# Kernel tuning notes

Hardware: AMD Instinct MI355X
Metric: run time of the kernel (lower is better)

Reference implementation:

```python
import jax, jax.numpy as jnp
import numpy as np

VOCAB, EMB, HID = 120000, 64, 128
B, T = 256, 512


def _rnn_layer(inp, W_ih, b_ih, W_hh, b_hh):
    # inp: [B,T,D]. PyTorch RNN: h_t = tanh(W_ih x_t + b_ih + W_hh h_{t-1} + b_hh)
    pre = jnp.einsum('btd,hd->bth', inp, W_ih) + b_ih + b_hh  # input part hoisted out of scan
    h0 = jnp.zeros((inp.shape[0], W_hh.shape[0]), inp.dtype)

    def step(h, p_t):
        h = jnp.tanh(p_t + h @ W_hh.T)
        return h, h

    hT, outs = jax.lax.scan(step, h0, pre.transpose(1, 0, 2))  # scan over time
    return outs.transpose(1, 0, 2), hT  # [B,T,H], [B,H]


def _layernorm(x, g, b, eps=1e-5):
    mu = jnp.mean(x, axis=-1, keepdims=True)
    var = jnp.var(x, axis=-1, keepdims=True)
    return (x - mu) * jax.lax.rsqrt(var + eps) * g + b


def setup_inputs() -> dict:
    key = jax.random.key(0)
    ks = jax.random.split(key, 10)
    emb = jax.random.normal(ks[0], (VOCAB, EMB), jnp.float32) * 0.02
    emb = emb.at[0].set(0.0)  # padding_idx=0
    s_in, s_h = 1.0 / np.sqrt(HID), 1.0 / np.sqrt(HID)
    return {
        'x': jax.random.randint(ks[1], (B, T), 0, VOCAB),
        'emb': emb,
        'W_ih1': jax.random.normal(ks[2], (HID, EMB), jnp.float32) * s_in,
        'b_ih1': jnp.zeros((HID,), jnp.float32),
        'W_hh1': jax.random.normal(ks[3], (HID, HID), jnp.float32) * s_h,
        'b_hh1': jnp.zeros((HID,), jnp.float32),
        'W_ih2': jax.random.normal(ks[4], (HID, HID), jnp.float32) * s_in,
        'b_ih2': jnp.zeros((HID,), jnp.float32),
        'W_hh2': jax.random.normal(ks[5], (HID, HID), jnp.float32) * s_h,
        'b_hh2': jnp.zeros((HID,), jnp.float32),
        'ln_g': jnp.ones((HID,), jnp.float32),
        'ln_b': jnp.zeros((HID,), jnp.float32),
        'proj_W': jax.random.normal(ks[6], (HID, HID), jnp.float32) * s_h,
        'proj_b': jnp.zeros((HID,), jnp.float32),
        'on_g': jnp.ones((HID,), jnp.float32),
        'on_b': jnp.zeros((HID,), jnp.float32),
    }


def reference(x, emb, W_ih1, b_ih1, W_hh1, b_hh1, W_ih2, b_ih2, W_hh2, b_hh2,
              ln_g, ln_b, proj_W, proj_b, on_g, on_b):
    e = emb[x]                                   # [B,T,64]
    out1, _ = _rnn_layer(e, W_ih1, b_ih1, W_hh1, b_hh1)   # dropout is identity in eval
    _, h2 = _rnn_layer(out1, W_ih2, b_ih2, W_hh2, b_hh2)  # h2: [B,128] (last hidden state)
    rep = _layernorm(h2, ln_g, ln_b)
    rep = jnp.tanh(rep @ proj_W.T + proj_b)
    rep = _layernorm(rep, on_g, on_b)
    return rep
```

## Files before the change

### kernel.cpp

```cpp
#include <hip/hip_runtime.h>

#define BT (256*512)
#define HID 128
#define EMB 64
#define CH 32

typedef _Float16 half2_t __attribute__((ext_vector_type(2)));

__device__ inline float fast_tanh(float x) {
    float e = __expf(2.f * x);
    return 1.f - __fdividef(2.f, e + 1.f);
}

#define OPQ(v) asm volatile("" : "+v"(v.x), "+v"(v.y), "+v"(v.z), "+v"(v.w))
#define W16PIN \
    OPQ(w0);OPQ(w1);OPQ(w2);OPQ(w3);OPQ(w4);OPQ(w5);OPQ(w6);OPQ(w7); \
    OPQ(w8);OPQ(w9);OPQ(w10);OPQ(w11);OPQ(w12);OPQ(w13);OPQ(w14);OPQ(w15);
#define WDUALLOAD \
    float4 w0=wr0[0],w1=wr0[1],w2=wr0[2],w3=wr0[3],w4=wr0[4],w5=wr0[5],w6=wr0[6],w7=wr0[7], \
           w8=wr1[0],w9=wr1[1],w10=wr1[2],w11=wr1[3],w12=wr1[4],w13=wr1[5],w14=wr1[6],w15=wr1[7];

#define DACC(n, m) { float4 hv = hp[n]; \
    a0=fmaf(hv.x,w##n.x,a0); a1=fmaf(hv.y,w##n.y,a1); \
    a2=fmaf(hv.z,w##n.z,a2); a3=fmaf(hv.w,w##n.w,a3); \
    c0=fmaf(hv.x,w##m.x,c0); c1=fmaf(hv.y,w##m.y,c1); \
    c2=fmaf(hv.z,w##m.z,c2); c3=fmaf(hv.w,w##m.w,c3); }
#define DACC8 DACC(0,8) DACC(1,9) DACC(2,10) DACC(3,11) \
              DACC(4,12) DACC(5,13) DACC(6,14) DACC(7,15)

#define BCH(u) __builtin_bit_cast(half2_t, u)
#define FMX2(qq, wa, wb, wc, wd) { \
    half2_t p0=BCH(qq.x), p1=BCH(qq.y), p2=BCH(qq.z), p3=BCH(qq.w); \
    float f0=(float)p0.x, f1=(float)p0.y, f2=(float)p1.x, f3=(float)p1.y, \
          f4=(float)p2.x, f5=(float)p2.y, f6=(float)p3.x, f7=(float)p3.y; \
    a0=fmaf(f0,wa.x,a0); a1=fmaf(f1,wa.y,a1); a2=fmaf(f2,wa.z,a2); a3=fmaf(f3,wa.w,a3); \
    a0=fmaf(f4,wb.x,a0); a1=fmaf(f5,wb.y,a1); a2=fmaf(f6,wb.z,a2); a3=fmaf(f7,wb.w,a3); \
    c0=fmaf(f0,wc.x,c0); c1=fmaf(f1,wc.y,c1); c2=fmaf(f2,wc.z,c2); c3=fmaf(f3,wc.w,c3); \
    c0=fmaf(f4,wd.x,c0); c1=fmaf(f5,wd.y,c1); c2=fmaf(f6,wd.z,c2); c3=fmaf(f7,wd.w,c3); }
#define DOT32H2(hsrc) \
    { uint4 q0h=hsrc[0],q1h=hsrc[1],q2h=hsrc[2],q3h=hsrc[3]; \
      FMX2(q0h,w0,w1,w8,w9) FMX2(q1h,w2,w3,w10,w11) \
      FMX2(q2h,w4,w5,w12,w13) FMX2(q3h,w6,w7,w14,w15) }

__global__ __launch_bounds__(256)
__attribute__((amdgpu_waves_per_eu(1, 2)))
void k_embed_pre1(
    const int* __restrict__ x, const float* __restrict__ emb,
    const float* __restrict__ Wih1, const float* __restrict__ bih1,
    const float* __restrict__ bhh1, float* __restrict__ pre1)
{
    __shared__ float sA[32][128];
    __shared__ float sW[32][132];
    __shared__ int stok[128];
    const int tid = threadIdx.x;
    const int base = blockIdx.x * 128;
    const int tx = tid & 15, ty = tid >> 4;
    const int ox = tx * 8, py = ty * 8;
    const int pl = tid & 127, half = tid >> 7;
    if (tid < 128) stok[tid] = x[base + tid];
    float acc[8][8];
#pragma unroll
    for (int p = 0; p < 8; ++p)
#pragma unroll
        for (int o = 0; o < 8; ++o) acc[p][o] = 0.f;
    __syncthreads();
    const float4* ws = (const float4*)(Wih1 + (size_t)pl * EMB + half * 16);
    const float4* as = (const float4*)(emb + (size_t)stok[pl] * EMB + half * 16);
    float4 qw[2][4], qe[2][4];
#pragma unroll
    for (int kc = 0; kc < 2; ++kc)
#pragma unroll
        for (int k = 0; k < 4; ++k) {
            qw[kc][k] = ws[kc * 8 + k];
            qe[kc][k] = as[kc * 8 + k];
        }
    for (int kc = 0; kc < 2; ++kc) {
        {
            const int jb = half * 16;
#pragma unroll
            for (int k = 0; k < 4; ++k) {
                float4 q = qw[kc][k], e = qe[kc][k];
                sW[jb + 4*k + 0][pl] = q.x; sW[jb + 4*k + 1][pl] = q.y;
                sW[jb + 4*k + 2][pl] = q.z; sW[jb + 4*k + 3][pl] = q.w;
                sA[jb + 4*k + 0][pl] = e.x; sA[jb + 4*k + 1][pl] = e.y;
                sA[jb + 4*k + 2][pl] = e.z; sA[jb + 4*k + 3][pl] = e.w;
            }
        }
        __syncthreads();
#pragma unroll 4
        for (int j = 0; j < 32; ++j) {
            float4 a0 = *(const float4*)&sA[j][py];
            float4 a1 = *(const float4*)&sA[j][py + 4];
            float4 b0 = *(const float4*)&sW[j][ox];
            float4 b1 = *(const float4*)&sW[j][ox + 4];
            float av[8] = {a0.x,a0.y,a0.z,a0.w,a1.x,a1.y,a1.z,a1.w};
            float bv[8] = {b0.x,b0.y,b0.z,b0.w,b1.x,b1.y,b1.z,b1.w};
#pragma unroll
            for (int p = 0; p < 8; ++p)
#pragma unroll
                for (int o = 0; o < 8; ++o)
                    acc[p][o] = fmaf(av[p], bv[o], acc[p][o]);
        }
        __syncthreads();
    }
    float bo[8];
#pragma unroll
    for (int o = 0; o < 8; ++o) bo[o] = bih1[ox + o] + bhh1[ox + o];
#pragma unroll
    for (int p = 0; p < 8; ++p) {
        float* cp = pre1 + (size_t)(base + py + p) * HID + ox;
        *(float4*)cp       = make_float4(acc[p][0]+bo[0], acc[p][1]+bo[1], acc[p][2]+bo[2], acc[p][3]+bo[3]);
        *(float4*)(cp + 4) = make_float4(acc[p][4]+bo[4], acc[p][5]+bo[5], acc[p][6]+bo[6], acc[p][7]+bo[7]);
    }
}

__device__ inline float bsum768(float v, volatile float* sc, int tid) {
#pragma unroll
    for (int off = 32; off > 0; off >>= 1) v += __shfl_down(v, off, 64);
    __syncthreads();
    if ((tid & 63) == 0) sc[tid >> 6] = v;
    __syncthreads();
    float s = 0.f;
#pragma unroll
    for (int k = 0; k < 12; ++k) s += sc[k];
    return s;
}

__global__ __launch_bounds__(768)
__attribute__((amdgpu_waves_per_eu(1, 3)))
void k_rnn_fused(
    const float* __restrict__ pre1, const float* __restrict__ Whh1,
    const float* __restrict__ Wih2, const float* __restrict__ bih2,
    const float* __restrict__ bhh2, const float* __restrict__ Whh2,
    const float* __restrict__ ln_g, const float* __restrict__ ln_b,
    const float* __restrict__ projW, const float* __restrict__ proj_b,
    const float* __restrict__ on_g, const float* __restrict__ on_b,
    float* __restrict__ out)
{
    __shared__ __align__(16) float    h1b[2][HID];
    __shared__ __align__(16) _Float16 h1h[2][HID];
    __shared__ __align__(16) float    h2b[2][HID];
    __shared__ __align__(16) float sp[3][4][HID];
    __shared__ __align__(16) float spre[CH * HID];
    __shared__ float sfin[HID];
    __shared__ float sc[12];
    const int b   = blockIdx.x;
    const int tid = threadIdx.x;
    const int g   = tid >> 8;
    const int gt  = tid & 255;
    const int q   = gt >> 6;
    const int r0  = gt & 63;
    const int i   = gt & 127;
    const float* wbase = (g == 0) ? Whh1 : ((g == 1) ? Wih2 : Whh2);
    const float4* wr0 = reinterpret_cast<const float4*>(wbase + (size_t)r0 * HID + q * 32);
    const float4* wr1 = reinterpret_cast<const float4*>(wbase + (size_t)(r0 + 64) * HID + q * 32);
    WDUALLOAD; W16PIN;
    const float bias2 = (g == 1) ? (bih2[i] + bhh2[i]) : 0.f;
    if (tid < 128) {
        h1b[0][tid] = 0.f; h1h[0][tid] = (_Float16)0.f; h2b[0][tid] = 0.f;
    }
    const float4* gsrc = reinterpret_cast<const float4*>(pre1 + (size_t)b * 512 * HID);
    float4*       spv  = reinterpret_cast<float4*>(spre);
    __syncthreads();
    for (int c = 0; c < 512 / CH; ++c) {
        if (tid < 512) {
            float4 rr0 = gsrc[c * 1024 + tid];
            float4 rr1 = gsrc[c * 1024 + tid + 512];
            spv[tid]       = rr0;
            spv[tid + 512] = rr1;
        }
        __syncthreads();
        for (int s = 0; s < CH; ++s) {
            const int t = c * CH + s;
            float a0 = 0, a1 = 0, a2 = 0, a3 = 0;
            float c0 = 0, c1 = 0, c2 = 0, c3 = 0;
            if (g == 1) {
                const uint4* hsrc = reinterpret_cast<const uint4*>(h1h[t & 1] + q * 32);
                DOT32H2(hsrc);
            } else {
                const float* hsel = (g == 0) ? h1b[t & 1] : h2b[t & 1];
                const float4* hp = reinterpret_cast<const float4*>(hsel + q * 32);
                DACC8;
            }
            sp[g][q][r0]      = (a0 + a1) + (a2 + a3);
            sp[g][q][r0 + 64] = (c0 + c1) + (c2 + c3);
            __syncthreads();
            if (tid < 128) {
                float hn = fast_tanh(spre[s * HID + i] +
                    ((sp[0][0][i] + sp[0][1][i]) + (sp[0][2][i] + sp[0][3][i])));
                h1b[(t + 1) & 1][i] = hn;
                h1h[(t + 1) & 1][i] = (_Float16)hn;
            } else if (g == 1 && gt < 128) {
                float v = bias2 +
                    ((sp[1][0][i] + sp[1][1][i]) + (sp[1][2][i] + sp[1][3][i])) +
                    ((sp[2][0][i] + sp[2][1][i]) + (sp[2][2][i] + sp[2][3][i]));
                h2b[(t + 1) & 1][i] = (t > 0) ? fast_tanh(v) : 0.f;
            }
            __syncthreads();
        }
    }
    {
        float a0 = 0, a1 = 0, a2 = 0, a3 = 0;
        float c0 = 0, c1 = 0, c2 = 0, c3 = 0;
        if (g == 1) {
            const uint4* hsrc = reinterpret_cast<const uint4*>(h1h[0] + q * 32);
            DOT32H2(hsrc);
            sp[1][q][r0]      = (a0 + a1) + (a2 + a3);
            sp[1][q][r0 + 64] = (c0 + c1) + (c2 + c3);
        } else if (g == 2) {
            const float4* hp = reinterpret_cast<const float4*>(h2b[0] + q * 32);
            DACC8;
            sp[2][q][r0]      = (a0 + a1) + (a2 + a3);
            sp[2][q][r0 + 64] = (c0 + c1) + (c2 + c3);
        }
    }
    __syncthreads();
    if (g == 1 && gt < 128)
        sfin[i] = fast_tanh(bias2 +
            ((sp[1][0][i] + sp[1][1][i]) + (sp[1][2][i] + sp[1][3][i])) +
            ((sp[2][0][i] + sp[2][1][i]) + (sp[2][2][i] + sp[2][3][i])));
    __syncthreads();
    float hn = (tid < 128) ? sfin[i] : 0.f;
    float s1 = bsum768(hn, sc, tid);
    float s2 = bsum768(hn * hn, sc, tid);
    float mu = s1 * (1.f / 128.f);
    float var = s2 * (1.f / 128.f) - mu * mu;
    __syncthreads();
    if (tid < 128) spre[i] = (hn - mu) * rsqrtf(var + 1e-5f) * ln_g[i] + ln_b[i];
    __syncthreads();
    float pv = 0.f;
    if (tid < 128) {
        float a0 = proj_b[i], a1 = 0, a2 = 0, a3 = 0;
        const float4* hp = reinterpret_cast<const float4*>(spre);
        const float4* pr = reinterpret_cast<const float4*>(projW + (size_t)i * HID);
#pragma unroll
        for (int k = 0; k < HID / 4; ++k) {
            float4 u = pr[k];
            float4 hv = hp[k];
            a0 = fmaf(hv.x, u.x, a0); a1 = fmaf(hv.y, u.y, a1);
            a2 = fmaf(hv.z, u.z, a2); a3 = fmaf(hv.w, u.w, a3);
        }
        pv = tanhf((a0 + a1) + (a2 + a3));
    }
    float t1 = bsum768(pv, sc, tid);
    float t2 = bsum768(pv * pv, sc, tid);
    float mu2 = t1 * (1.f / 128.f);
    float var2 = t2 * (1.f / 128.f) - mu2 * mu2;
    if (tid < 128)
        out[(size_t)b * HID + i] = (pv - mu2) * rsqrtf(var2 + 1e-5f) * on_g[i] + on_b[i];
}

extern "C" void kernel_launch(void* const* d_in, const int* in_sizes, int n_in,
                              void* d_out, int out_size, void* d_ws, size_t ws_size,
                              hipStream_t stream)
{
    const int*   x     = (const int*)  d_in[0];
    const float* emb   = (const float*)d_in[1];
    const float* Wih1  = (const float*)d_in[2];
    const float* bih1  = (const float*)d_in[3];
    const float* Whh1  = (const float*)d_in[4];
    const float* bhh1  = (const float*)d_in[5];
    const float* Wih2  = (const float*)d_in[6];
    const float* bih2  = (const float*)d_in[7];
    const float* Whh2  = (const float*)d_in[8];
    const float* bhh2  = (const float*)d_in[9];
    const float* ln_g  = (const float*)d_in[10];
    const float* ln_b  = (const float*)d_in[11];
    const float* projW = (const float*)d_in[12];
    const float* projb = (const float*)d_in[13];
    const float* on_g  = (const float*)d_in[14];
    const float* on_b  = (const float*)d_in[15];

    float* pre1 = (float*)d_ws;

    k_embed_pre1<<<BT / 128, 256, 0, stream>>>(x, emb, Wih1, bih1, bhh1, pre1);
    k_rnn_fused<<<256, 768, 0, stream>>>(pre1, Whh1, Wih2, bih2, bhh2, Whh2,
                                         ln_g, ln_b, projW, projb, on_g, on_b,
                                         (float*)d_out);
}
```

Measured before the change: 485.0 us.

## Restructure fused RNN kernel to 3 waves with in-register dot reductions via DPP

Shrinks the recurrent kernel from 768 threads to 192 (three waves). Each lane now holds 8 weight rows by 32 columns in registers and uses packed FP32 FMA, with DPP and swizzle cross-lane reductions replacing the shared-memory partial-sum buffer. This removes one of the two block barriers per timestep, prefetches the next pre1 chunk into registers while the current one is consumed, and drops the FP16 h1 copy so everything stays in fp32. The epilogue layernorm and projection now run in a single wave using shuffles. The cost is a very high register footprint of 256 weight VGPRs per lane, and only three waves per CU with little latency hiding.

```diff
diff --git a/kernel.cpp b/kernel.cpp
--- a/kernel.cpp
+++ b/kernel.cpp
@@ -5,42 +5,22 @@
 #define EMB 64
 #define CH 32
 
-typedef _Float16 half2_t __attribute__((ext_vector_type(2)));
-
-__device__ inline float fast_tanh(float x) {
+typedef float f32x2 __attribute__((ext_vector_type(2)));
+
+__device__ __forceinline__ float fast_tanh(float x) {
     float e = __expf(2.f * x);
     return 1.f - __fdividef(2.f, e + 1.f);
 }
 
-#define OPQ(v) asm volatile("" : "+v"(v.x), "+v"(v.y), "+v"(v.z), "+v"(v.w))
-#define W16PIN \
-    OPQ(w0);OPQ(w1);OPQ(w2);OPQ(w3);OPQ(w4);OPQ(w5);OPQ(w6);OPQ(w7); \
-    OPQ(w8);OPQ(w9);OPQ(w10);OPQ(w11);OPQ(w12);OPQ(w13);OPQ(w14);OPQ(w15);
-#define WDUALLOAD \
-    float4 w0=wr0[0],w1=wr0[1],w2=wr0[2],w3=wr0[3],w4=wr0[4],w5=wr0[5],w6=wr0[6],w7=wr0[7], \
-           w8=wr1[0],w9=wr1[1],w10=wr1[2],w11=wr1[3],w12=wr1[4],w13=wr1[5],w14=wr1[6],w15=wr1[7];
-
-#define DACC(n, m) { float4 hv = hp[n]; \
-    a0=fmaf(hv.x,w##n.x,a0); a1=fmaf(hv.y,w##n.y,a1); \
-    a2=fmaf(hv.z,w##n.z,a2); a3=fmaf(hv.w,w##n.w,a3); \
-    c0=fmaf(hv.x,w##m.x,c0); c1=fmaf(hv.y,w##m.y,c1); \
-    c2=fmaf(hv.z,w##m.z,c2); c3=fmaf(hv.w,w##m.w,c3); }
-#define DACC8 DACC(0,8) DACC(1,9) DACC(2,10) DACC(3,11) \
-              DACC(4,12) DACC(5,13) DACC(6,14) DACC(7,15)
-
-#define BCH(u) __builtin_bit_cast(half2_t, u)
-#define FMX2(qq, wa, wb, wc, wd) { \
-    half2_t p0=BCH(qq.x), p1=BCH(qq.y), p2=BCH(qq.z), p3=BCH(qq.w); \
-    float f0=(float)p0.x, f1=(float)p0.y, f2=(float)p1.x, f3=(float)p1.y, \
-          f4=(float)p2.x, f5=(float)p2.y, f6=(float)p3.x, f7=(float)p3.y; \
-    a0=fmaf(f0,wa.x,a0); a1=fmaf(f1,wa.y,a1); a2=fmaf(f2,wa.z,a2); a3=fmaf(f3,wa.w,a3); \
-    a0=fmaf(f4,wb.x,a0); a1=fmaf(f5,wb.y,a1); a2=fmaf(f6,wb.z,a2); a3=fmaf(f7,wb.w,a3); \
-    c0=fmaf(f0,wc.x,c0); c1=fmaf(f1,wc.y,c1); c2=fmaf(f2,wc.z,c2); c3=fmaf(f3,wc.w,c3); \
-    c0=fmaf(f4,wd.x,c0); c1=fmaf(f5,wd.y,c1); c2=fmaf(f6,wd.z,c2); c3=fmaf(f7,wd.w,c3); }
-#define DOT32H2(hsrc) \
-    { uint4 q0h=hsrc[0],q1h=hsrc[1],q2h=hsrc[2],q3h=hsrc[3]; \
-      FMX2(q0h,w0,w1,w8,w9) FMX2(q1h,w2,w3,w10,w11) \
-      FMX2(q2h,w4,w5,w12,w13) FMX2(q3h,w6,w7,w14,w15) }
+#define PKFMA(d, a, b) asm("v_pk_fma_f32 %0, %1, %2, %0" : "+v"(d) : "v"(a), "v"(b))
+#define DPPADD(v, ctrl) ((v) + __int_as_float(__builtin_amdgcn_mov_dpp(__float_as_int(v), (ctrl), 0xf, 0xf, false)))
+#define SWZ4(v) __int_as_float(__builtin_amdgcn_ds_swizzle(__float_as_int(v), 0x101F))
+
+__device__ __forceinline__ float mux4(int k, float x0, float x1, float x2, float x3) {
+    float t0 = (k & 1) ? x1 : x0;
+    float t1 = (k & 1) ? x3 : x2;
+    return (k & 2) ? t1 : t0;
+}
 
 __global__ __launch_bounds__(256)
 __attribute__((amdgpu_waves_per_eu(1, 2)))
@@ -114,20 +94,8 @@
     }
 }
 
-__device__ inline float bsum768(float v, volatile float* sc, int tid) {
-#pragma unroll
-    for (int off = 32; off > 0; off >>= 1) v += __shfl_down(v, off, 64);
-    __syncthreads();
-    if ((tid & 63) == 0) sc[tid >> 6] = v;
-    __syncthreads();
-    float s = 0.f;
-#pragma unroll
-    for (int k = 0; k < 12; ++k) s += sc[k];
-    return s;
-}
-
-__global__ __launch_bounds__(768)
-__attribute__((amdgpu_waves_per_eu(1, 3)))
+__global__ __launch_bounds__(192, 1)
+__attribute__((amdgpu_waves_per_eu(1, 1)))
 void k_rnn_fused(
     const float* __restrict__ pre1, const float* __restrict__ Whh1,
     const float* __restrict__ Wih2, const float* __restrict__ bih2,
@@ -137,117 +105,166 @@
     const float* __restrict__ on_g, const float* __restrict__ on_b,
     float* __restrict__ out)
 {
-    __shared__ __align__(16) float    h1b[2][HID];
-    __shared__ __align__(16) _Float16 h1h[2][HID];
-    __shared__ __align__(16) float    h2b[2][HID];
-    __shared__ __align__(16) float sp[3][4][HID];
+    __shared__ __align__(16) float hb[2][2][144];
     __shared__ __align__(16) float spre[CH * HID];
-    __shared__ float sfin[HID];
-    __shared__ float sc[12];
-    const int b   = blockIdx.x;
-    const int tid = threadIdx.x;
-    const int g   = tid >> 8;
-    const int gt  = tid & 255;
-    const int q   = gt >> 6;
-    const int r0  = gt & 63;
-    const int i   = gt & 127;
-    const float* wbase = (g == 0) ? Whh1 : ((g == 1) ? Wih2 : Whh2);
-    const float4* wr0 = reinterpret_cast<const float4*>(wbase + (size_t)r0 * HID + q * 32);
-    const float4* wr1 = reinterpret_cast<const float4*>(wbase + (size_t)(r0 + 64) * HID + q * 32);
-    WDUALLOAD; W16PIN;
-    const float bias2 = (g == 1) ? (bih2[i] + bhh2[i]) : 0.f;
-    if (tid < 128) {
-        h1b[0][tid] = 0.f; h1h[0][tid] = (_Float16)0.f; h2b[0][tid] = 0.f;
-    }
-    const float4* gsrc = reinterpret_cast<const float4*>(pre1 + (size_t)b * 512 * HID);
-    float4*       spv  = reinterpret_cast<float4*>(spre);
+    __shared__ __align__(16) float sfin[HID];
+
+    const int bb   = blockIdx.x;
+    const int tid  = threadIdx.x;
+    const int wid  = tid >> 6;
+    const int lane = tid & 63;
+    const int lq   = lane & 3;
+    const int lo4  = lane & 4;
+
+    int rowbase, layer;
+    const float* wsel;
+    if (wid == 0) { rowbase = (lane >> 2) * 8; layer = 0; wsel = Whh1; }
+    else {
+        rowbase = ((wid - 1) * 8 + (lane >> 3)) * 8;
+        layer = lo4 ? 1 : 0;
+        wsel = lo4 ? Whh2 : Wih2;
+    }
+    const int own0 = rowbase + ((wid == 0) ? lq : (lane & 7));
+    const int own1 = own0 + 4;
+
+    f32x2 W2[8][16];
+#pragma unroll
+    for (int r = 0; r < 8; ++r) {
+        const f32x2* src = (const f32x2*)(wsel + (size_t)(rowbase + r) * HID + lq * 32);
+#pragma unroll
+        for (int k = 0; k < 16; ++k) W2[r][k] = src[k];
+    }
+#pragma unroll
+    for (int r = 0; r < 8; ++r)
+#pragma unroll
+        for (int k = 0; k < 16; ++k) asm volatile("" : "+v"(W2[r][k]));
+
+    const float b2o = (wid != 0) ? (bih2[own0] + bhh2[own0]) : 0.f;
+
+    if (tid < 144) { hb[0][0][tid] = 0.f; hb[0][1][tid] = 0.f; }
+
+    const f32x2* r_e = (const f32x2*)&hb[0][layer][lq * 36];
+    const f32x2* r_o = (const f32x2*)&hb[1][layer][lq * 36];
+    const int wl = (wid == 0) ? 0 : 1;
+    float* w_e0 = &hb[1][wl][((own0 >> 5) * 36) + (own0 & 31)];
+    float* w_o0 = &hb[0][wl][((own0 >> 5) * 36) + (own0 & 31)];
+    float* w_e1 = &hb[1][0][((own1 >> 5) * 36) + (own1 & 31)];
+    float* w_o1 = &hb[0][0][((own1 >> 5) * 36) + (own1 & 31)];
+
+    const float4* gsrc = (const float4*)(pre1 + (size_t)bb * 512 * HID);
+    float4* spv = (float4*)spre;
+    float4 pf0, pf1, pf2, pf3, pf4, pf5;
+
+    auto prefetch = [&](int cc) {
+        const int base = cc * 1024;
+        pf0 = gsrc[base + tid];
+        pf1 = gsrc[base + tid + 192];
+        pf2 = gsrc[base + tid + 384];
+        pf3 = gsrc[base + tid + 576];
+        pf4 = gsrc[base + tid + 768];
+        if (wid == 2) pf5 = gsrc[base + lane + 960];
+    };
+
+    auto do_step = [&](int t, int sic, const f32x2* __restrict__ hp,
+                       float* wp0, float* wp1) {
+        float pA = 0.f, pB = 0.f;
+        if (wid == 0) {
+            pA = spre[sic * HID + own0];
+            pB = spre[sic * HID + own1];
+        }
+        f32x2 a0={0.f,0.f}, a1={0.f,0.f}, a2={0.f,0.f}, a3={0.f,0.f},
+              a4={0.f,0.f}, a5={0.f,0.f}, a6={0.f,0.f}, a7={0.f,0.f};
+#pragma unroll
+        for (int kk = 0; kk < 16; ++kk) {
+            f32x2 hv = hp[kk];
+            PKFMA(a0, hv, W2[0][kk]); PKFMA(a1, hv, W2[1][kk]);
+            PKFMA(a2, hv, W2[2][kk]); PKFMA(a3, hv, W2[3][kk]);
+            PKFMA(a4, hv, W2[4][kk]); PKFMA(a5, hv, W2[5][kk]);
+            PKFMA(a6, hv, W2[6][kk]); PKFMA(a7, hv, W2[7][kk]);
+        }
+        float s0 = a0.x + a0.y, s1 = a1.x + a1.y, s2 = a2.x + a2.y, s3 = a3.x + a3.y,
+              s4 = a4.x + a4.y, s5 = a5.x + a5.y, s6 = a6.x + a6.y, s7 = a7.x + a7.y;
+        s0 = DPPADD(s0, 0xB1); s1 = DPPADD(s1, 0xB1); s2 = DPPADD(s2, 0xB1); s3 = DPPADD(s3, 0xB1);
+        s4 = DPPADD(s4, 0xB1); s5 = DPPADD(s5, 0xB1); s6 = DPPADD(s6, 0xB1); s7 = DPPADD(s7, 0xB1);
+        s0 = DPPADD(s0, 0x4E); s1 = DPPADD(s1, 0x4E); s2 = DPPADD(s2, 0x4E); s3 = DPPADD(s3, 0x4E);
+        s4 = DPPADD(s4, 0x4E); s5 = DPPADD(s5, 0x4E); s6 = DPPADD(s6, 0x4E); s7 = DPPADD(s7, 0x4E);
+        if (wid == 0) {
+            float v0 = mux4(lq, s0, s1, s2, s3);
+            float v1 = mux4(lq, s4, s5, s6, s7);
+            *wp0 = fast_tanh(pA + v0);
+            *wp1 = fast_tanh(pB + v1);
+        } else {
+            float mql = mux4(lq, s0, s1, s2, s3);
+            float mqh = mux4(lq, s4, s5, s6, s7);
+            float m1 = lo4 ? mqh : mql;
+            float m2 = lo4 ? mql : mqh;
+            float bv = b2o + m1 + SWZ4(m2);
+            *wp0 = (t > 0) ? fast_tanh(bv) : 0.f;
+        }
+    };
+
+    prefetch(0);
     __syncthreads();
+
+#pragma unroll 1
     for (int c = 0; c < 512 / CH; ++c) {
-        if (tid < 512) {
-            float4 rr0 = gsrc[c * 1024 + tid];
-            float4 rr1 = gsrc[c * 1024 + tid + 512];
-            spv[tid]       = rr0;
-            spv[tid + 512] = rr1;
-        }
+        spv[tid] = pf0; spv[tid + 192] = pf1; spv[tid + 384] = pf2;
+        spv[tid + 576] = pf3; spv[tid + 768] = pf4;
+        if (wid == 2) spv[lane + 960] = pf5;
         __syncthreads();
-        for (int s = 0; s < CH; ++s) {
-            const int t = c * CH + s;
-            float a0 = 0, a1 = 0, a2 = 0, a3 = 0;
-            float c0 = 0, c1 = 0, c2 = 0, c3 = 0;
-            if (g == 1) {
-                const uint4* hsrc = reinterpret_cast<const uint4*>(h1h[t & 1] + q * 32);
-                DOT32H2(hsrc);
-            } else {
-                const float* hsel = (g == 0) ? h1b[t & 1] : h2b[t & 1];
-                const float4* hp = reinterpret_cast<const float4*>(hsel + q * 32);
-                DACC8;
-            }
-            sp[g][q][r0]      = (a0 + a1) + (a2 + a3);
-            sp[g][q][r0 + 64] = (c0 + c1) + (c2 + c3);
+        if (c < 512 / CH - 1) prefetch(c + 1);
+        const int t0 = c * CH;
+#pragma unroll 1
+        for (int s = 0; s < CH; s += 2) {
+            do_step(t0 + s,     s,     r_e, w_e0, w_e1);
             __syncthreads();
-            if (tid < 128) {
-                float hn = fast_tanh(spre[s * HID + i] +
-                    ((sp[0][0][i] + sp[0][1][i]) + (sp[0][2][i] + sp[0][3][i])));
-                h1b[(t + 1) & 1][i] = hn;
-                h1h[(t + 1) & 1][i] = (_Float16)hn;
-            } else if (g == 1 && gt < 128) {
-                float v = bias2 +
-                    ((sp[1][0][i] + sp[1][1][i]) + (sp[1][2][i] + sp[1][3][i])) +
-                    ((sp[2][0][i] + sp[2][1][i]) + (sp[2][2][i] + sp[2][3][i]));
-                h2b[(t + 1) & 1][i] = (t > 0) ? fast_tanh(v) : 0.f;
-            }
+            do_step(t0 + s + 1, s + 1, r_o, w_o0, w_o1);
             __syncthreads();
         }
     }
+
     {
-        float a0 = 0, a1 = 0, a2 = 0, a3 = 0;
-        float c0 = 0, c1 = 0, c2 = 0, c3 = 0;
-        if (g == 1) {
-            const uint4* hsrc = reinterpret_cast<const uint4*>(h1h[0] + q * 32);
-            DOT32H2(hsrc);
-            sp[1][q][r0]      = (a0 + a1) + (a2 + a3);
-            sp[1][q][r0 + 64] = (c0 + c1) + (c2 + c3);
-        } else if (g == 2) {
-            const float4* hp = reinterpret_cast<const float4*>(h2b[0] + q * 32);
-            DACC8;
-            sp[2][q][r0]      = (a0 + a1) + (a2 + a3);
-            sp[2][q][r0 + 64] = (c0 + c1) + (c2 + c3);
-        }
+        float* d0 = (wid == 0) ? w_e0 : &sfin[own0];
+        do_step(512, 0, r_e, d0, w_e1);
     }
     __syncthreads();
-    if (g == 1 && gt < 128)
-        sfin[i] = fast_tanh(bias2 +
-            ((sp[1][0][i] + sp[1][1][i]) + (sp[1][2][i] + sp[1][3][i])) +
-            ((sp[2][0][i] + sp[2][1][i]) + (sp[2][2][i] + sp[2][3][i])));
-    __syncthreads();
-    float hn = (tid < 128) ? sfin[i] : 0.f;
-    float s1 = bsum768(hn, sc, tid);
-    float s2 = bsum768(hn * hn, sc, tid);
-    float mu = s1 * (1.f / 128.f);
-    float var = s2 * (1.f / 128.f) - mu * mu;
-    __syncthreads();
-    if (tid < 128) spre[i] = (hn - mu) * rsqrtf(var + 1e-5f) * ln_g[i] + ln_b[i];
-    __syncthreads();
-    float pv = 0.f;
-    if (tid < 128) {
-        float a0 = proj_b[i], a1 = 0, a2 = 0, a3 = 0;
-        const float4* hp = reinterpret_cast<const float4*>(spre);
-        const float4* pr = reinterpret_cast<const float4*>(projW + (size_t)i * HID);
-#pragma unroll
-        for (int k = 0; k < HID / 4; ++k) {
-            float4 u = pr[k];
-            float4 hv = hp[k];
-            a0 = fmaf(hv.x, u.x, a0); a1 = fmaf(hv.y, u.y, a1);
-            a2 = fmaf(hv.z, u.z, a2); a3 = fmaf(hv.w, u.w, a3);
-        }
-        pv = tanhf((a0 + a1) + (a2 + a3));
-    }
-    float t1 = bsum768(pv, sc, tid);
-    float t2 = bsum768(pv * pv, sc, tid);
-    float mu2 = t1 * (1.f / 128.f);
-    float var2 = t2 * (1.f / 128.f) - mu2 * mu2;
-    if (tid < 128)
-        out[(size_t)b * HID + i] = (pv - mu2) * rsqrtf(var2 + 1e-5f) * on_g[i] + on_b[i];
+
+    if (wid == 0) {
+        float v0 = sfin[lane], v1 = sfin[lane + 64];
+        float sa = v0 + v1, sb = v0 * v0 + v1 * v1;
+#pragma unroll
+        for (int k = 32; k > 0; k >>= 1) { sa += __shfl_xor(sa, k); sb += __shfl_xor(sb, k); }
+        float mu  = sa * (1.f / 128.f);
+        float var = sb * (1.f / 128.f) - mu * mu;
+        float rs  = rsqrtf(var + 1e-5f);
+        float n0 = (v0 - mu) * rs * ln_g[lane] + ln_b[lane];
+        float n1 = (v1 - mu) * rs * ln_g[lane + 64] + ln_b[lane + 64];
+        sfin[lane] = n0; sfin[lane + 64] = n1;
+        asm volatile("s_waitcnt lgkmcnt(0)" ::: "memory");
+        float A0 = proj_b[lane],      A1 = 0.f, A2 = 0.f, A3 = 0.f;
+        float C0 = proj_b[lane + 64], C1 = 0.f, C2 = 0.f, C3 = 0.f;
+        const float4* hp4 = (const float4*)sfin;
+        const float4* p0 = (const float4*)(projW + (size_t)lane * HID);
+        const float4* p1 = (const float4*)(projW + (size_t)(lane + 64) * HID);
+#pragma unroll
+        for (int k = 0; k < 32; ++k) {
+            float4 h4 = hp4[k], u = p0[k], w = p1[k];
+            A0 = fmaf(h4.x, u.x, A0); A1 = fmaf(h4.y, u.y, A1);
+            A2 = fmaf(h4.z, u.z, A2); A3 = fmaf(h4.w, u.w, A3);
+            C0 = fmaf(h4.x, w.x, C0); C1 = fmaf(h4.y, w.y, C1);
+            C2 = fmaf(h4.z, w.z, C2); C3 = fmaf(h4.w, w.w, C3);
+        }
+        float pv0 = tanhf((A0 + A1) + (A2 + A3));
+        float pv1 = tanhf((C0 + C1) + (C2 + C3));
+        float ta = pv0 + pv1, tb = pv0 * pv0 + pv1 * pv1;
+#pragma unroll
+        for (int k = 32; k > 0; k >>= 1) { ta += __shfl_xor(ta, k); tb += __shfl_xor(tb, k); }
+        float mu2  = ta * (1.f / 128.f);
+        float var2 = tb * (1.f / 128.f) - mu2 * mu2;
+        float rs2  = rsqrtf(var2 + 1e-5f);
+        out[(size_t)bb * HID + lane]      = (pv0 - mu2) * rs2 * on_g[lane] + on_b[lane];
+        out[(size_t)bb * HID + lane + 64] = (pv1 - mu2) * rs2 * on_g[lane + 64] + on_b[lane + 64];
+    }
 }
 
 extern "C" void kernel_launch(void* const* d_in, const int* in_sizes, int n_in,
@@ -274,7 +291,7 @@
     float* pre1 = (float*)d_ws;
 
     k_embed_pre1<<<BT / 128, 256, 0, stream>>>(x, emb, Wih1, bih1, bhh1, pre1);
-    k_rnn_fused<<<256, 768, 0, stream>>>(pre1, Whh1, Wih2, bih2, bhh2, Whh2,
+    k_rnn_fused<<<256, 192, 0, stream>>>(pre1, Whh1, Wih2, bih2, bhh2, Whh2,
                                          ln_g, ln_b, projW, projb, on_g, on_b,
                                          (float*)d_out);
 }
```

Result: slower. 571.3 us (+17.8%).

## Reduce recurrent matvec partials with DPP and drop one barrier per step

Applied to the files above, without the earlier changes.

Restructures the fused two-layer RNN recurrence so each wave splits the hidden dimension across 8 lanes. Partial dot products are reduced within the wave using DPP moves instead of writing them to shared memory and summing them after an extra barrier. Each step now needs one __syncthreads instead of two, and the next pre-activation chunk is prefetched into registers while the current chunk is processed. The shared-state layout is padded, and the fp16 copy of h1 is removed. The risks are higher register pressure, plus the chance that the DPP row-control reductions across lane groups or the padded indexing are subtly wrong.

```diff
diff --git a/kernel.cpp b/kernel.cpp
--- a/kernel.cpp
+++ b/kernel.cpp
@@ -5,42 +5,24 @@
 #define EMB 64
 #define CH 32
 
-typedef _Float16 half2_t __attribute__((ext_vector_type(2)));
-
-__device__ inline float fast_tanh(float x) {
+__device__ __forceinline__ float fast_tanh(float x) {
     float e = __expf(2.f * x);
     return 1.f - __fdividef(2.f, e + 1.f);
 }
 
 #define OPQ(v) asm volatile("" : "+v"(v.x), "+v"(v.y), "+v"(v.z), "+v"(v.w))
-#define W16PIN \
-    OPQ(w0);OPQ(w1);OPQ(w2);OPQ(w3);OPQ(w4);OPQ(w5);OPQ(w6);OPQ(w7); \
-    OPQ(w8);OPQ(w9);OPQ(w10);OPQ(w11);OPQ(w12);OPQ(w13);OPQ(w14);OPQ(w15);
-#define WDUALLOAD \
-    float4 w0=wr0[0],w1=wr0[1],w2=wr0[2],w3=wr0[3],w4=wr0[4],w5=wr0[5],w6=wr0[6],w7=wr0[7], \
-           w8=wr1[0],w9=wr1[1],w10=wr1[2],w11=wr1[3],w12=wr1[4],w13=wr1[5],w14=wr1[6],w15=wr1[7];
-
-#define DACC(n, m) { float4 hv = hp[n]; \
-    a0=fmaf(hv.x,w##n.x,a0); a1=fmaf(hv.y,w##n.y,a1); \
-    a2=fmaf(hv.z,w##n.z,a2); a3=fmaf(hv.w,w##n.w,a3); \
-    c0=fmaf(hv.x,w##m.x,c0); c1=fmaf(hv.y,w##m.y,c1); \
-    c2=fmaf(hv.z,w##m.z,c2); c3=fmaf(hv.w,w##m.w,c3); }
-#define DACC8 DACC(0,8) DACC(1,9) DACC(2,10) DACC(3,11) \
-              DACC(4,12) DACC(5,13) DACC(6,14) DACC(7,15)
-
-#define BCH(u) __builtin_bit_cast(half2_t, u)
-#define FMX2(qq, wa, wb, wc, wd) { \
-    half2_t p0=BCH(qq.x), p1=BCH(qq.y), p2=BCH(qq.z), p3=BCH(qq.w); \
-    float f0=(float)p0.x, f1=(float)p0.y, f2=(float)p1.x, f3=(float)p1.y, \
-          f4=(float)p2.x, f5=(float)p2.y, f6=(float)p3.x, f7=(float)p3.y; \
-    a0=fmaf(f0,wa.x,a0); a1=fmaf(f1,wa.y,a1); a2=fmaf(f2,wa.z,a2); a3=fmaf(f3,wa.w,a3); \
-    a0=fmaf(f4,wb.x,a0); a1=fmaf(f5,wb.y,a1); a2=fmaf(f6,wb.z,a2); a3=fmaf(f7,wb.w,a3); \
-    c0=fmaf(f0,wc.x,c0); c1=fmaf(f1,wc.y,c1); c2=fmaf(f2,wc.z,c2); c3=fmaf(f3,wc.w,c3); \
-    c0=fmaf(f4,wd.x,c0); c1=fmaf(f5,wd.y,c1); c2=fmaf(f6,wd.z,c2); c3=fmaf(f7,wd.w,c3); }
-#define DOT32H2(hsrc) \
-    { uint4 q0h=hsrc[0],q1h=hsrc[1],q2h=hsrc[2],q3h=hsrc[3]; \
-      FMX2(q0h,w0,w1,w8,w9) FMX2(q1h,w2,w3,w10,w11) \
-      FMX2(q2h,w4,w5,w12,w13) FMX2(q3h,w6,w7,w14,w15) }
+
+#define DPPADD(v, ctrl) ((v) + __int_as_float(__builtin_amdgcn_mov_dpp(__float_as_int(v), (ctrl), 0xF, 0xF, false)))
+
+#define RACC(P, Q, wa, wb, wc, wd) \
+    P = fmaf(hv0.x, wa.x, P); Q = fmaf(hv0.y, wa.y, Q); \
+    P = fmaf(hv0.z, wa.z, P); Q = fmaf(hv0.w, wa.w, Q); \
+    P = fmaf(hv1.x, wb.x, P); Q = fmaf(hv1.y, wb.y, Q); \
+    P = fmaf(hv1.z, wb.z, P); Q = fmaf(hv1.w, wb.w, Q); \
+    P = fmaf(hv2.x, wc.x, P); Q = fmaf(hv2.y, wc.y, Q); \
+    P = fmaf(hv2.z, wc.z, P); Q = fmaf(hv2.w, wc.w, Q); \
+    P = fmaf(hv3.x, wd.x, P); Q = fmaf(hv3.y, wd.y, Q); \
+    P = fmaf(hv3.z, wd.z, P); Q = fmaf(hv3.w, wd.w, Q);
 
 __global__ __launch_bounds__(256)
 __attribute__((amdgpu_waves_per_eu(1, 2)))
@@ -137,102 +119,115 @@
     const float* __restrict__ on_g, const float* __restrict__ on_b,
     float* __restrict__ out)
 {
-    __shared__ __align__(16) float    h1b[2][HID];
-    __shared__ __align__(16) _Float16 h1h[2][HID];
-    __shared__ __align__(16) float    h2b[2][HID];
-    __shared__ __align__(16) float sp[3][4][HID];
+    __shared__ __align__(16) float h1[2][160];
+    __shared__ __align__(16) float h2[2][160];
     __shared__ __align__(16) float spre[CH * HID];
     __shared__ float sfin[HID];
     __shared__ float sc[12];
-    const int b   = blockIdx.x;
-    const int tid = threadIdx.x;
-    const int g   = tid >> 8;
-    const int gt  = tid & 255;
-    const int q   = gt >> 6;
-    const int r0  = gt & 63;
-    const int i   = gt & 127;
-    const float* wbase = (g == 0) ? Whh1 : ((g == 1) ? Wih2 : Whh2);
-    const float4* wr0 = reinterpret_cast<const float4*>(wbase + (size_t)r0 * HID + q * 32);
-    const float4* wr1 = reinterpret_cast<const float4*>(wbase + (size_t)(r0 + 64) * HID + q * 32);
-    WDUALLOAD; W16PIN;
-    const float bias2 = (g == 1) ? (bih2[i] + bhh2[i]) : 0.f;
-    if (tid < 128) {
-        h1b[0][tid] = 0.f; h1h[0][tid] = (_Float16)0.f; h2b[0][tid] = 0.f;
-    }
-    const float4* gsrc = reinterpret_cast<const float4*>(pre1 + (size_t)b * 512 * HID);
-    float4*       spv  = reinterpret_cast<float4*>(spre);
-    __syncthreads();
+
+    const int bb   = blockIdx.x;
+    const int tid  = threadIdx.x;
+    const int w    = tid >> 6;
+    const int lane = tid & 63;
+    const bool L1  = (w < 4);
+    const int  e   = lane & 7;
+    const int  m   = L1 ? 0 : ((lane >> 3) & 1);
+    const int  rg  = L1 ? (lane >> 3) : (lane >> 4);
+    const int  rowbase = L1 ? (32 * w + rg) : (16 * (w - 4) + rg);
+    const int  rstep   = L1 ? 8 : 4;
+    const float* wmat  = L1 ? Whh1 : (m ? Whh2 : Wih2);
+
+    const float4* wr0 = (const float4*)(wmat + (size_t)(rowbase            ) * HID + e * 16);
+    const float4* wr1 = (const float4*)(wmat + (size_t)(rowbase +     rstep) * HID + e * 16);
+    const float4* wr2 = (const float4*)(wmat + (size_t)(rowbase + 2 * rstep) * HID + e * 16);
+    const float4* wr3 = (const float4*)(wmat + (size_t)(rowbase + 3 * rstep) * HID + e * 16);
+    float4 w0 = wr0[0], w1 = wr0[1], w2  = wr0[2], w3  = wr0[3],
+           w4 = wr1[0], w5 = wr1[1], w6  = wr1[2], w7  = wr1[3],
+           w8 = wr2[0], w9 = wr2[1], w10 = wr2[2], w11 = wr2[3],
+           w12= wr3[0], w13= wr3[1], w14 = wr3[2], w15 = wr3[3];
+    OPQ(w0);OPQ(w1);OPQ(w2);OPQ(w3);OPQ(w4);OPQ(w5);OPQ(w6);OPQ(w7);
+    OPQ(w8);OPQ(w9);OPQ(w10);OPQ(w11);OPQ(w12);OPQ(w13);OPQ(w14);OPQ(w15);
+
+    const bool wr_en = L1 ? (e < 4) : (m == 0 && e < 4);
+    const int  wrow  = rowbase + (e & 3) * rstep;
+    const int  wword = ((wrow >> 4) * 20) + (wrow & 15);
+    const float b2w  = (!L1 && wr_en) ? (bih2[wrow] + bhh2[wrow]) : 0.f;
+
+    if (tid < 160) { h1[0][tid] = 0.f; h2[0][tid] = 0.f; }
+
+    const float* srcb = (L1 || m == 0) ? &h1[0][0] : &h2[0][0];
+    const float4* rp0 = (const float4*)(srcb + e * 20);
+    const float4* rp1 = (const float4*)(srcb + 160 + e * 20);
+    float* dstb = L1 ? &h1[0][0] : &h2[0][0];
+    float* wp_e = dstb + 160 + wword;
+    float* wp_o = dstb + wword;
+
+    const float4* gsrc = (const float4*)(pre1 + (size_t)bb * 512 * HID);
+    float4* spv = (float4*)spre;
+    float4 pf0, pf1;
+    if (tid < 512) { pf0 = gsrc[tid]; pf1 = gsrc[tid + 512]; }
+    __syncthreads();
+
+    auto do_step = [&](int t, int s, const float4* rp, float* wpt) {
+        float4 hv0 = rp[0], hv1 = rp[1], hv2 = rp[2], hv3 = rp[3];
+        float p0=0,q0=0,p1=0,q1=0,p2=0,q2=0,p3=0,q3=0;
+        RACC(p0,q0, w0,w1,w2,w3)
+        RACC(p1,q1, w4,w5,w6,w7)
+        RACC(p2,q2, w8,w9,w10,w11)
+        RACC(p3,q3, w12,w13,w14,w15)
+        float s0 = p0+q0, s1 = p1+q1, s2 = p2+q2, s3 = p3+q3;
+        s0 = DPPADD(s0, 0xB1); s1 = DPPADD(s1, 0xB1); s2 = DPPADD(s2, 0xB1); s3 = DPPADD(s3, 0xB1);
+        s0 = DPPADD(s0, 0x4E); s1 = DPPADD(s1, 0x4E); s2 = DPPADD(s2, 0x4E); s3 = DPPADD(s3, 0x4E);
+        s0 = DPPADD(s0, 0x141); s1 = DPPADD(s1, 0x141); s2 = DPPADD(s2, 0x141); s3 = DPPADD(s3, 0x141);
+        if (!L1) {
+            s0 = DPPADD(s0, 0x140); s1 = DPPADD(s1, 0x140);
+            s2 = DPPADD(s2, 0x140); s3 = DPPADD(s3, 0x140);
+        }
+        if (wr_en) {
+            float ta = (e & 1) ? s1 : s0;
+            float tb = (e & 1) ? s3 : s2;
+            float v  = (e & 2) ? tb : ta;
+            if (L1) *wpt = fast_tanh(spre[s * HID + wrow] + v);
+            else    *wpt = (t > 0) ? fast_tanh(b2w + v) : 0.f;
+        }
+        __syncthreads();
+    };
+
+#pragma unroll 1
     for (int c = 0; c < 512 / CH; ++c) {
-        if (tid < 512) {
-            float4 rr0 = gsrc[c * 1024 + tid];
-            float4 rr1 = gsrc[c * 1024 + tid + 512];
-            spv[tid]       = rr0;
-            spv[tid + 512] = rr1;
-        }
-        __syncthreads();
-        for (int s = 0; s < CH; ++s) {
-            const int t = c * CH + s;
-            float a0 = 0, a1 = 0, a2 = 0, a3 = 0;
-            float c0 = 0, c1 = 0, c2 = 0, c3 = 0;
-            if (g == 1) {
-                const uint4* hsrc = reinterpret_cast<const uint4*>(h1h[t & 1] + q * 32);
-                DOT32H2(hsrc);
-            } else {
-                const float* hsel = (g == 0) ? h1b[t & 1] : h2b[t & 1];
-                const float4* hp = reinterpret_cast<const float4*>(hsel + q * 32);
-                DACC8;
-            }
-            sp[g][q][r0]      = (a0 + a1) + (a2 + a3);
-            sp[g][q][r0 + 64] = (c0 + c1) + (c2 + c3);
-            __syncthreads();
-            if (tid < 128) {
-                float hn = fast_tanh(spre[s * HID + i] +
-                    ((sp[0][0][i] + sp[0][1][i]) + (sp[0][2][i] + sp[0][3][i])));
-                h1b[(t + 1) & 1][i] = hn;
-                h1h[(t + 1) & 1][i] = (_Float16)hn;
-            } else if (g == 1 && gt < 128) {
-                float v = bias2 +
-                    ((sp[1][0][i] + sp[1][1][i]) + (sp[1][2][i] + sp[1][3][i])) +
-                    ((sp[2][0][i] + sp[2][1][i]) + (sp[2][2][i] + sp[2][3][i]));
-                h2b[(t + 1) & 1][i] = (t > 0) ? fast_tanh(v) : 0.f;
-            }
-            __syncthreads();
-        }
-    }
+        if (tid < 512) { spv[tid] = pf0; spv[tid + 512] = pf1; }
+        __syncthreads();
+        if (c < 512 / CH - 1 && tid < 512) {
+            pf0 = gsrc[(c + 1) * 1024 + tid];
+            pf1 = gsrc[(c + 1) * 1024 + tid + 512];
+        }
+        const int t0 = c * CH;
+#pragma unroll 1
+        for (int s = 0; s < CH; s += 2) {
+            do_step(t0 + s,     s,     rp0, wp_e);
+            do_step(t0 + s + 1, s + 1, rp1, wp_o);
+        }
+    }
+
     {
-        float a0 = 0, a1 = 0, a2 = 0, a3 = 0;
-        float c0 = 0, c1 = 0, c2 = 0, c3 = 0;
-        if (g == 1) {
-            const uint4* hsrc = reinterpret_cast<const uint4*>(h1h[0] + q * 32);
-            DOT32H2(hsrc);
-            sp[1][q][r0]      = (a0 + a1) + (a2 + a3);
-            sp[1][q][r0 + 64] = (c0 + c1) + (c2 + c3);
-        } else if (g == 2) {
-            const float4* hp = reinterpret_cast<const float4*>(h2b[0] + q * 32);
-            DACC8;
-            sp[2][q][r0]      = (a0 + a1) + (a2 + a3);
-            sp[2][q][r0 + 64] = (c0 + c1) + (c2 + c3);
-        }
-    }
-    __syncthreads();
-    if (g == 1 && gt < 128)
-        sfin[i] = fast_tanh(bias2 +
-            ((sp[1][0][i] + sp[1][1][i]) + (sp[1][2][i] + sp[1][3][i])) +
-            ((sp[2][0][i] + sp[2][1][i]) + (sp[2][2][i] + sp[2][3][i])));
-    __syncthreads();
+        float* wpD = L1 ? wp_e : &sfin[wrow];
+        do_step(512, 0, rp0, wpD);
+    }
+
+    const int i = tid & 127;
     float hn = (tid < 128) ? sfin[i] : 0.f;
-    float s1 = bsum768(hn, sc, tid);
-    float s2 = bsum768(hn * hn, sc, tid);
-    float mu = s1 * (1.f / 128.f);
-    float var = s2 * (1.f / 128.f) - mu * mu;
+    float s1v = bsum768(hn, sc, tid);
+    float s2v = bsum768(hn * hn, sc, tid);
+    float mu = s1v * (1.f / 128.f);
+    float var = s2v * (1.f / 128.f) - mu * mu;
     __syncthreads();
     if (tid < 128) spre[i] = (hn - mu) * rsqrtf(var + 1e-5f) * ln_g[i] + ln_b[i];
     __syncthreads();
     float pv = 0.f;
     if (tid < 128) {
         float a0 = proj_b[i], a1 = 0, a2 = 0, a3 = 0;
-        const float4* hp = reinterpret_cast<const float4*>(spre);
-        const float4* pr = reinterpret_cast<const float4*>(projW + (size_t)i * HID);
+        const float4* hp = (const float4*)spre;
+        const float4* pr = (const float4*)(projW + (size_t)i * HID);
 #pragma unroll
         for (int k = 0; k < HID / 4; ++k) {
             float4 u = pr[k];
@@ -247,7 +242,7 @@
     float mu2 = t1 * (1.f / 128.f);
     float var2 = t2 * (1.f / 128.f) - mu2 * mu2;
     if (tid < 128)
-        out[(size_t)b * HID + i] = (pv - mu2) * rsqrtf(var2 + 1e-5f) * on_g[i] + on_b[i];
+        out[(size_t)bb * HID + i] = (pv - mu2) * rsqrtf(var2 + 1e-5f) * on_g[i] + on_b[i];
 }
 
 extern "C" void kernel_launch(void* const* d_in, const int* in_sizes, int n_in,
```

After: 447.9 us. 1.08x faster.
